# Optimization experiments

Measured on AMD Instinct MI355X. Metric: run time of the kernel, lower is better.

The kernel has to match this reference:

```python
import jax, jax.numpy as jnp
import numpy as np


def setup_inputs() -> dict:
    key = jax.random.key(0)
    x = jax.random.normal(key, (256, 64, 4096), dtype=jnp.float32)
    return {"x": x}


def _mat_shrinkage(cov, n):
    # cov: [B, p, p]; Rao-Blackwell Ledoit-Wolf shrinkage toward scaled identity
    p = cov.shape[-1]
    I = jnp.eye(p, dtype=cov.dtype)[None]                      # [1, p, p]
    trace = jnp.trace(cov, axis1=-2, axis2=-1)[:, None, None]  # [B, 1, 1]
    F_hat = trace / p * I                                      # [B, p, p]
    # tr(C @ C) without materializing C@C
    second_trace = jnp.einsum('bij,bji->b', cov, cov)[:, None, None]
    numerator = (n - 2) / n * second_trace + trace ** 2
    denominator = (n + 2) * (second_trace - trace ** 2 / p)
    rho = jnp.minimum(numerator / denominator, 1.0)
    return rho * F_hat + (1.0 - rho) * cov


def reference(x):
    # x: [B, C, M]
    B, C, M = x.shape
    x_mu = jnp.mean(x, axis=2, keepdims=True)          # [B, C, 1]
    x_cnt = x - x_mu                                    # [B, C, M]
    cov = jnp.einsum('bcm,bdm->bcd', x_cnt, x_cnt) / M  # [B, C, C]
    cov = _mat_shrinkage(cov, n=M)
    L = jnp.linalg.cholesky(jnp.linalg.inv(cov))        # [B, C, C], lower
    # Z = L^T @ x_cnt
    Z = jnp.einsum('bdc,bdm->bcm', L, x_cnt)            # [B, C, M]
    return Z
```

## Files before the change

### kernel.cpp

```cpp
#include <hip/hip_runtime.h>

#define B_ 256
#define C_ 64
#define M_ 4096

__global__ __launch_bounds__(256) void k_fused(const float* __restrict__ x,
                                               float* __restrict__ out) {
    const int b = blockIdx.x;
    const int t = threadIdx.x;
    const int w = t >> 6;
    const int l = t & 63;

    __shared__ float St[64][68];
    __shared__ float Cw[64][68];
    __shared__ float Ww[64][68];
    __shared__ float ms[64][17];
    __shared__ float mu[64];
    __shared__ float red[256];
    __shared__ float ucol[64];
    __shared__ float wmu[64];
    __shared__ float sc[4];

    const float* xb = x + (size_t)b * (C_ * M_);
    float* ob = out + (size_t)b * (C_ * M_);

    const int tc = l >> 3, td = l & 7;
    const int cl = l >> 2;
    const int m4 = l & 3;

    float acc[8][8];
#pragma unroll
    for (int i = 0; i < 8; ++i)
#pragma unroll
        for (int j = 0; j < 8; ++j) acc[i][j] = 0.f;
    float msum[4] = {0.f, 0.f, 0.f, 0.f};

    const int mbase = w * 1024;
    float4 r[4];
#pragma unroll
    for (int k = 0; k < 4; ++k)
        r[k] = *(const float4*)(xb + (size_t)(cl + 16 * k) * M_ + mbase + m4 * 4);

    for (int s = 0; s < 64; ++s) {
        __syncthreads();
#pragma unroll
        for (int k = 0; k < 4; ++k) {
            float4 v = r[k];
            msum[k] += v.x + v.y + v.z + v.w;
            const int row = w * 16 + m4 * 4;
            const int c = cl + 16 * k;
            St[row + 0][c] = v.x;
            St[row + 1][c] = v.y;
            St[row + 2][c] = v.z;
            St[row + 3][c] = v.w;
        }
        if (s < 63) {
#pragma unroll
            for (int k = 0; k < 4; ++k)
                r[k] = *(const float4*)(xb + (size_t)(cl + 16 * k) * M_ +
                                        mbase + (s + 1) * 16 + m4 * 4);
        }
        __syncthreads();
#pragma unroll 2
        for (int m = 0; m < 16; ++m) {
            float a[8], bb[8];
            *(float4*)&a[0]  = *(const float4*)&St[w * 16 + m][tc * 8];
            *(float4*)&a[4]  = *(const float4*)&St[w * 16 + m][tc * 8 + 4];
            *(float4*)&bb[0] = *(const float4*)&St[w * 16 + m][td * 8];
            *(float4*)&bb[4] = *(const float4*)&St[w * 16 + m][td * 8 + 4];
#pragma unroll
            for (int i = 0; i < 8; ++i)
#pragma unroll
                for (int j = 0; j < 8; ++j)
                    acc[i][j] = fmaf(a[i], bb[j], acc[i][j]);
        }
    }
#pragma unroll
    for (int k = 0; k < 4; ++k) ms[cl + 16 * k][w * 4 + m4] = msum[k];
    __syncthreads();

    if (w == 1) {
#pragma unroll
        for (int i = 0; i < 8; ++i) {
            *(float4*)&Ww[tc * 8 + i][td * 8]     = make_float4(acc[i][0], acc[i][1], acc[i][2], acc[i][3]);
            *(float4*)&Ww[tc * 8 + i][td * 8 + 4] = make_float4(acc[i][4], acc[i][5], acc[i][6], acc[i][7]);
        }
        float s = 0.f;
#pragma unroll
        for (int q = 0; q < 16; ++q) s += ms[l][q];
        mu[l] = s * (1.0f / M_);
    } else if (w == 2) {
#pragma unroll
        for (int i = 0; i < 8; ++i) {
            *(float4*)&Cw[tc * 8 + i][td * 8]     = make_float4(acc[i][0], acc[i][1], acc[i][2], acc[i][3]);
            *(float4*)&Cw[tc * 8 + i][td * 8 + 4] = make_float4(acc[i][4], acc[i][5], acc[i][6], acc[i][7]);
        }
    } else if (w == 3) {
#pragma unroll
        for (int i = 0; i < 8; ++i) {
            *(float4*)&St[tc * 8 + i][td * 8]     = make_float4(acc[i][0], acc[i][1], acc[i][2], acc[i][3]);
            *(float4*)&St[tc * 8 + i][td * 8 + 4] = make_float4(acc[i][4], acc[i][5], acc[i][6], acc[i][7]);
        }
    }
    __syncthreads();
    if (w == 0) {
#pragma unroll
        for (int i = 0; i < 8; ++i) {
            float4 p0 = *(const float4*)&Ww[tc * 8 + i][td * 8];
            float4 p1 = *(const float4*)&Cw[tc * 8 + i][td * 8];
            float4 p2 = *(const float4*)&St[tc * 8 + i][td * 8];
            float4 q0 = *(const float4*)&Ww[tc * 8 + i][td * 8 + 4];
            float4 q1 = *(const float4*)&Cw[tc * 8 + i][td * 8 + 4];
            float4 q2 = *(const float4*)&St[tc * 8 + i][td * 8 + 4];
            float4 lo = make_float4(acc[i][0] + p0.x + p1.x + p2.x,
                                    acc[i][1] + p0.y + p1.y + p2.y,
                                    acc[i][2] + p0.z + p1.z + p2.z,
                                    acc[i][3] + p0.w + p1.w + p2.w);
            float4 hi = make_float4(acc[i][4] + q0.x + q1.x + q2.x,
                                    acc[i][5] + q0.y + q1.y + q2.y,
                                    acc[i][6] + q0.z + q1.z + q2.z,
                                    acc[i][7] + q0.w + q1.w + q2.w);
            *(float4*)&Cw[tc * 8 + i][td * 8]     = lo;
            *(float4*)&Cw[tc * 8 + i][td * 8 + 4] = hi;
        }
    }
    __syncthreads();
    for (int idx = t; idx < 4096; idx += 256) {
        int i = idx >> 6, j = idx & 63;
        Cw[i][j] = Cw[i][j] * (1.0f / M_) - mu[i] * mu[j];
    }
    __syncthreads();

    {
        float trp = 0.f, stp = 0.f;
        for (int idx = t; idx < 4096; idx += 256) {
            int i = idx >> 6, j = idx & 63;
            float v = Cw[i][j];
            stp = fmaf(v, Cw[j][i], stp);
            if (i == j) trp += v;
        }
        red[t] = stp;
        __syncthreads();
        for (int off = 128; off > 0; off >>= 1) {
            if (t < off) red[t] += red[t + off];
            __syncthreads();
        }
        if (t == 0) sc[1] = red[0];
        __syncthreads();
        red[t] = trp;
        __syncthreads();
        for (int off = 128; off > 0; off >>= 1) {
            if (t < off) red[t] += red[t + off];
            __syncthreads();
        }
        if (t == 0) {
            float tr = red[0], st = sc[1];
            const float n = (float)M_, p = 64.f;
            float num = (n - 2.f) / n * st + tr * tr;
            float den = (n + 2.f) * (st - tr * tr / p);
            float rho = fminf(num / den, 1.0f);
            sc[0] = tr;
            sc[2] = rho;
        }
        __syncthreads();
        float rho = sc[2], tr = sc[0];
        float dadd = rho * tr * (1.0f / 64.0f);
        for (int idx = t; idx < 4096; idx += 256) {
            int i = idx >> 6, j = idx & 63;
            float v = (1.f - rho) * Cw[i][j];
            if (i == j) v += dadd;
            Cw[i][j] = v;
        }
    }

    for (int k = 63; k >= 0; --k) {
        __syncthreads();
        float dkk = sqrtf(Cw[k][k]);
        float dinv = 1.0f / dkk;
        for (int i = t; i < k; i += 256) ucol[i] = Cw[i][k] * dinv;
        if (t == 0) ucol[k] = dkk;
        __syncthreads();
        const int nel = (k * (k + 1)) >> 1;
        for (int e = t; e < nel; e += 256) {
            int j = (int)((sqrtf((float)(8 * e + 1)) - 1.0f) * 0.5f);
            if (e < ((j * (j + 1)) >> 1)) --j;
            else if (e >= (((j + 1) * (j + 2)) >> 1)) ++j;
            int i = e - ((j * (j + 1)) >> 1);
            Cw[i][j] = fmaf(-ucol[i], ucol[j], Cw[i][j]);
        }
        for (int i = t; i <= k; i += 256) Cw[i][k] = ucol[i];
    }
    __syncthreads();

    if (t < 64) {
        const int j = t;
        Ww[j][j] = 1.0f / Cw[j][j];
        for (int i = j - 1; i >= 0; --i) {
            float s0 = 0.f, s1 = 0.f;
            int lq = i + 1;
            for (; lq + 1 <= j; lq += 2) {
                s0 = fmaf(Cw[i][lq], Ww[lq][j], s0);
                s1 = fmaf(Cw[i][lq + 1], Ww[lq + 1][j], s1);
            }
            if (lq <= j) s0 = fmaf(Cw[i][lq], Ww[lq][j], s0);
            Ww[i][j] = -(s0 + s1) / Cw[i][i];
        }
    }
    __syncthreads();
    if (t < 64) {
        float s = 0.f;
        for (int d = t; d < 64; ++d) s = fmaf(Ww[t][d], mu[d], s);
        wmu[t] = s;
    }
    for (int idx = t; idx < 4096; idx += 256) {
        int d = idx >> 6, c = idx & 63;
        Cw[d][c] = (d >= c) ? Ww[c][d] : 0.f;
    }

    const int tc5 = t >> 5;
    const int tm5 = t & 31;
    const int cld = t >> 4;
    const int m45 = t & 15;
    const int d0 = w * 16;

    float4 r2[4];
#pragma unroll
    for (int k = 0; k < 4; ++k)
        r2[k] = *(const float4*)(xb + (size_t)(cld + 16 * k) * M_ + m45 * 4);

    for (int ch = 0; ch < 64; ++ch) {
        const int m0 = ch * 64;
        __syncthreads();
#pragma unroll
        for (int k = 0; k < 4; ++k)
            *(float4*)&St[cld + 16 * k][m45 * 4] = r2[k];
        if (ch < 63) {
#pragma unroll
            for (int k = 0; k < 4; ++k)
                r2[k] = *(const float4*)(xb + (size_t)(cld + 16 * k) * M_ +
                                         m0 + 64 + m45 * 4);
        }
        __syncthreads();
        float a2[8][2];
#pragma unroll
        for (int i = 0; i < 8; ++i) a2[i][0] = a2[i][1] = 0.f;
        for (int d = d0; d < 64; ++d) {
            float a[8];
            *(float4*)&a[0] = *(const float4*)&Cw[d][tc5 * 8];
            *(float4*)&a[4] = *(const float4*)&Cw[d][tc5 * 8 + 4];
            float2 bv = *(const float2*)&St[d][tm5 * 2];
#pragma unroll
            for (int i = 0; i < 8; ++i) {
                a2[i][0] = fmaf(a[i], bv.x, a2[i][0]);
                a2[i][1] = fmaf(a[i], bv.y, a2[i][1]);
            }
        }
#pragma unroll
        for (int i = 0; i < 8; ++i) {
            const int c = tc5 * 8 + i;
            float wv = wmu[c];
            float2 o = make_float2(a2[i][0] - wv, a2[i][1] - wv);
            *(float2*)(ob + (size_t)c * M_ + m0 + tm5 * 2) = o;
        }
    }
}

extern "C" void kernel_launch(void* const* d_in, const int* in_sizes, int n_in,
                              void* d_out, int out_size, void* d_ws, size_t ws_size,
                              hipStream_t stream) {
    const float* x = (const float*)d_in[0];
    float* out = (float*)d_out;
    k_fused<<<dim3(B_), 256, 0, stream>>>(x, out);
}
```

Before: 798.8 us.

## Split fused kernel into gram, cholesky and apply kernels with M-split parallelism

Replaces the single per-batch fused kernel with three kernels. The first computes raw Gram matrices and row sums over four M-slices per batch. The second reduces the slices, applies shrinkage, factors the matrix and inverts it. The third applies the triangular transform across four M-slices. This raises the grid from 256 blocks to 1024 blocks for the heavy phases so more CUs are busy, at the cost of a workspace round-trip, reading x twice and two extra launches. It also uses the uncentered Gram minus the mean outer product and folds the mean subtraction into a W·mu correction, which may lose some precision.

Result: faster. 749.2 us (-6.2%).

```diff
diff --git a/kernel.cpp b/kernel.cpp
--- a/kernel.cpp
+++ b/kernel.cpp
@@ -3,6 +3,340 @@
 #define B_ 256
 #define C_ 64
 #define M_ 4096
+#define S_ 4
+#define GSTRIDE 4160
+
+__global__ __launch_bounds__(256, 4) void k_gram(const float* __restrict__ x,
+                                                 float* __restrict__ wsA) {
+    const int b = blockIdx.x;
+    const int s = blockIdx.y;
+    const int t = threadIdx.x;
+    const int w = t >> 6;
+    const int l = t & 63;
+
+    __shared__ float St[64][68];
+    __shared__ float Bu[64][68];
+    __shared__ float ms[64][17];
+
+    const float* xb = x + (size_t)b * (C_ * M_);
+    float* g = wsA + (size_t)(b * S_ + s) * GSTRIDE;
+
+    const int tc = l >> 3, td = l & 7;
+    const int cl = l >> 2;
+    const int m4 = l & 3;
+
+    float acc[8][8];
+#pragma unroll
+    for (int i = 0; i < 8; ++i)
+#pragma unroll
+        for (int j = 0; j < 8; ++j) acc[i][j] = 0.f;
+    float msum[4] = {0.f, 0.f, 0.f, 0.f};
+
+    const int mbase = s * 1024 + w * 256;
+    float4 r[4];
+#pragma unroll
+    for (int k = 0; k < 4; ++k)
+        r[k] = *(const float4*)(xb + (size_t)(cl + 16 * k) * M_ + mbase + m4 * 4);
+
+    for (int st = 0; st < 16; ++st) {
+        __syncthreads();
+#pragma unroll
+        for (int k = 0; k < 4; ++k) {
+            float4 v = r[k];
+            msum[k] += v.x + v.y + v.z + v.w;
+            const int row = w * 16 + m4 * 4;
+            const int c = cl + 16 * k;
+            St[row + 0][c] = v.x;
+            St[row + 1][c] = v.y;
+            St[row + 2][c] = v.z;
+            St[row + 3][c] = v.w;
+        }
+        if (st < 15) {
+#pragma unroll
+            for (int k = 0; k < 4; ++k)
+                r[k] = *(const float4*)(xb + (size_t)(cl + 16 * k) * M_ +
+                                        mbase + (st + 1) * 16 + m4 * 4);
+        }
+        __syncthreads();
+#pragma unroll 2
+        for (int m = 0; m < 16; ++m) {
+            float a[8], bb[8];
+            *(float4*)&a[0]  = *(const float4*)&St[w * 16 + m][tc * 8];
+            *(float4*)&a[4]  = *(const float4*)&St[w * 16 + m][tc * 8 + 4];
+            *(float4*)&bb[0] = *(const float4*)&St[w * 16 + m][td * 8];
+            *(float4*)&bb[4] = *(const float4*)&St[w * 16 + m][td * 8 + 4];
+#pragma unroll
+            for (int i = 0; i < 8; ++i)
+#pragma unroll
+                for (int j = 0; j < 8; ++j)
+                    acc[i][j] = fmaf(a[i], bb[j], acc[i][j]);
+        }
+    }
+#pragma unroll
+    for (int k = 0; k < 4; ++k) ms[cl + 16 * k][w * 4 + m4] = msum[k];
+    __syncthreads();
+
+    if (w == 1) {
+#pragma unroll
+        for (int i = 0; i < 8; ++i) {
+            *(float4*)&St[tc * 8 + i][td * 8]     = make_float4(acc[i][0], acc[i][1], acc[i][2], acc[i][3]);
+            *(float4*)&St[tc * 8 + i][td * 8 + 4] = make_float4(acc[i][4], acc[i][5], acc[i][6], acc[i][7]);
+        }
+    } else if (w == 3) {
+#pragma unroll
+        for (int i = 0; i < 8; ++i) {
+            *(float4*)&Bu[tc * 8 + i][td * 8]     = make_float4(acc[i][0], acc[i][1], acc[i][2], acc[i][3]);
+            *(float4*)&Bu[tc * 8 + i][td * 8 + 4] = make_float4(acc[i][4], acc[i][5], acc[i][6], acc[i][7]);
+        }
+    }
+    __syncthreads();
+    if (w == 0) {
+#pragma unroll
+        for (int i = 0; i < 8; ++i) {
+            float4 p = *(const float4*)&St[tc * 8 + i][td * 8];
+            float4 q = *(const float4*)&St[tc * 8 + i][td * 8 + 4];
+            acc[i][0] += p.x; acc[i][1] += p.y; acc[i][2] += p.z; acc[i][3] += p.w;
+            acc[i][4] += q.x; acc[i][5] += q.y; acc[i][6] += q.z; acc[i][7] += q.w;
+        }
+    } else if (w == 2) {
+#pragma unroll
+        for (int i = 0; i < 8; ++i) {
+            float4 p = *(const float4*)&Bu[tc * 8 + i][td * 8];
+            float4 q = *(const float4*)&Bu[tc * 8 + i][td * 8 + 4];
+            acc[i][0] += p.x; acc[i][1] += p.y; acc[i][2] += p.z; acc[i][3] += p.w;
+            acc[i][4] += q.x; acc[i][5] += q.y; acc[i][6] += q.z; acc[i][7] += q.w;
+        }
+    }
+    __syncthreads();
+    if (w == 2) {
+#pragma unroll
+        for (int i = 0; i < 8; ++i) {
+            *(float4*)&St[tc * 8 + i][td * 8]     = make_float4(acc[i][0], acc[i][1], acc[i][2], acc[i][3]);
+            *(float4*)&St[tc * 8 + i][td * 8 + 4] = make_float4(acc[i][4], acc[i][5], acc[i][6], acc[i][7]);
+        }
+    }
+    __syncthreads();
+    if (w == 0) {
+#pragma unroll
+        for (int i = 0; i < 8; ++i) {
+            float4 p = *(const float4*)&St[tc * 8 + i][td * 8];
+            float4 q = *(const float4*)&St[tc * 8 + i][td * 8 + 4];
+            float4 lo = make_float4(acc[i][0] + p.x, acc[i][1] + p.y,
+                                    acc[i][2] + p.z, acc[i][3] + p.w);
+            float4 hi = make_float4(acc[i][4] + q.x, acc[i][5] + q.y,
+                                    acc[i][6] + q.z, acc[i][7] + q.w);
+            *(float4*)(g + (size_t)(tc * 8 + i) * 64 + td * 8)     = lo;
+            *(float4*)(g + (size_t)(tc * 8 + i) * 64 + td * 8 + 4) = hi;
+        }
+    } else if (w == 1) {
+        float sum = 0.f;
+#pragma unroll
+        for (int q = 0; q < 16; ++q) sum += ms[l][q];
+        g[4096 + l] = sum;
+    }
+}
+
+__global__ __launch_bounds__(256) void k_chol(const float* __restrict__ wsA,
+                                              float* __restrict__ wsB) {
+    const int b = blockIdx.x;
+    const int t = threadIdx.x;
+
+    __shared__ float Cw[64][68];
+    __shared__ float Ww[64][68];
+    __shared__ float mu[64];
+    __shared__ float red[256];
+    __shared__ float ucol[64];
+    __shared__ float sc[4];
+
+    const float* pa = wsA + (size_t)b * S_ * GSTRIDE;
+    float* o = wsB + (size_t)b * GSTRIDE;
+
+    for (int idx = t; idx < 4096; idx += 256) {
+        float v = 0.f;
+#pragma unroll
+        for (int s = 0; s < S_; ++s) v += pa[(size_t)s * GSTRIDE + idx];
+        Cw[idx >> 6][idx & 63] = v;
+    }
+    if (t < 64) {
+        float v = 0.f;
+#pragma unroll
+        for (int s = 0; s < S_; ++s) v += pa[(size_t)s * GSTRIDE + 4096 + t];
+        mu[t] = v * (1.0f / M_);
+    }
+    __syncthreads();
+    for (int idx = t; idx < 4096; idx += 256) {
+        int i = idx >> 6, j = idx & 63;
+        Cw[i][j] = Cw[i][j] * (1.0f / M_) - mu[i] * mu[j];
+    }
+    __syncthreads();
+
+    {
+        float trp = 0.f, stp = 0.f;
+        for (int idx = t; idx < 4096; idx += 256) {
+            int i = idx >> 6, j = idx & 63;
+            float v = Cw[i][j];
+            stp = fmaf(v, Cw[j][i], stp);
+            if (i == j) trp += v;
+        }
+        red[t] = stp;
+        __syncthreads();
+        for (int off = 128; off > 0; off >>= 1) {
+            if (t < off) red[t] += red[t + off];
+            __syncthreads();
+        }
+        if (t == 0) sc[1] = red[0];
+        __syncthreads();
+        red[t] = trp;
+        __syncthreads();
+        for (int off = 128; off > 0; off >>= 1) {
+            if (t < off) red[t] += red[t + off];
+            __syncthreads();
+        }
+        if (t == 0) {
+            float tr = red[0], st = sc[1];
+            const float n = (float)M_, p = 64.f;
+            float num = (n - 2.f) / n * st + tr * tr;
+            float den = (n + 2.f) * (st - tr * tr / p);
+            float rho = fminf(num / den, 1.0f);
+            sc[0] = tr;
+            sc[2] = rho;
+        }
+        __syncthreads();
+        float rho = sc[2], tr = sc[0];
+        float dadd = rho * tr * (1.0f / 64.0f);
+        for (int idx = t; idx < 4096; idx += 256) {
+            int i = idx >> 6, j = idx & 63;
+            float v = (1.f - rho) * Cw[i][j];
+            if (i == j) v += dadd;
+            Cw[i][j] = v;
+        }
+    }
+
+    for (int k = 63; k >= 0; --k) {
+        __syncthreads();
+        float dkk = sqrtf(Cw[k][k]);
+        float dinv = 1.0f / dkk;
+        for (int i = t; i < k; i += 256) ucol[i] = Cw[i][k] * dinv;
+        if (t == 0) ucol[k] = dkk;
+        __syncthreads();
+        const int nel = (k * (k + 1)) >> 1;
+        for (int e = t; e < nel; e += 256) {
+            int j = (int)((sqrtf((float)(8 * e + 1)) - 1.0f) * 0.5f);
+            if (e < ((j * (j + 1)) >> 1)) --j;
+            else if (e >= (((j + 1) * (j + 2)) >> 1)) ++j;
+            int i = e - ((j * (j + 1)) >> 1);
+            Cw[i][j] = fmaf(-ucol[i], ucol[j], Cw[i][j]);
+        }
+        for (int i = t; i <= k; i += 256) Cw[i][k] = ucol[i];
+    }
+    __syncthreads();
+
+    if (t < 64) {
+        const int j = t;
+        Ww[j][j] = 1.0f / Cw[j][j];
+        for (int i = j - 1; i >= 0; --i) {
+            float s0 = 0.f, s1 = 0.f;
+            int lq = i + 1;
+            for (; lq + 1 <= j; lq += 2) {
+                s0 = fmaf(Cw[i][lq], Ww[lq][j], s0);
+                s1 = fmaf(Cw[i][lq + 1], Ww[lq + 1][j], s1);
+            }
+            if (lq <= j) s0 = fmaf(Cw[i][lq], Ww[lq][j], s0);
+            Ww[i][j] = -(s0 + s1) / Cw[i][i];
+        }
+    }
+    __syncthreads();
+    if (t < 64) {
+        float s = 0.f;
+        for (int d = t; d < 64; ++d) s = fmaf(Ww[t][d], mu[d], s);
+        o[4096 + t] = s;
+    }
+    for (int idx = t; idx < 4096; idx += 256) {
+        int d = idx >> 6, c = idx & 63;
+        o[idx] = (d >= c) ? Ww[c][d] : 0.f;
+    }
+}
+
+__global__ __launch_bounds__(256, 4) void k_apply(const float* __restrict__ x,
+                                                  const float* __restrict__ wsB,
+                                                  float* __restrict__ out) {
+    const int b = blockIdx.x;
+    const int s = blockIdx.y;
+    const int t = threadIdx.x;
+    const int w = t >> 6;
+
+    __shared__ float Wt[64][68];
+    __shared__ float St[64][68];
+    __shared__ float wmu[64];
+
+    const float* xb = x + (size_t)b * (C_ * M_);
+    float* ob = out + (size_t)b * (C_ * M_);
+    const float* wsb = wsB + (size_t)b * GSTRIDE;
+
+    for (int idx = t; idx < 4096; idx += 256) Wt[idx >> 6][idx & 63] = wsb[idx];
+    if (t < 64) wmu[t] = wsb[4096 + t];
+
+    const int tc5 = t >> 4;
+    const int tm5 = t & 15;
+    const int cld = t >> 4;
+    const int m45 = t & 15;
+    const int d0 = w * 16;
+    const int mbase = s * 1024;
+
+    float4 r2[4];
+#pragma unroll
+    for (int k = 0; k < 4; ++k)
+        r2[k] = *(const float4*)(xb + (size_t)(cld + 16 * k) * M_ + mbase + m45 * 4);
+
+    for (int ch = 0; ch < 16; ++ch) {
+        const int m0 = mbase + ch * 64;
+        __syncthreads();
+#pragma unroll
+        for (int k = 0; k < 4; ++k)
+            *(float4*)&St[cld + 16 * k][m45 * 4] = r2[k];
+        if (ch < 15) {
+#pragma unroll
+            for (int k = 0; k < 4; ++k)
+                r2[k] = *(const float4*)(xb + (size_t)(cld + 16 * k) * M_ +
+                                         m0 + 64 + m45 * 4);
+        }
+        __syncthreads();
+        float a2[4][4];
+#pragma unroll
+        for (int i = 0; i < 4; ++i)
+#pragma unroll
+            for (int j = 0; j < 4; ++j) a2[i][j] = 0.f;
+#pragma unroll 2
+        for (int d = d0; d < 64; ++d) {
+            float4 a  = *(const float4*)&Wt[d][tc5 * 4];
+            float4 bv = *(const float4*)&St[d][tm5 * 4];
+            a2[0][0] = fmaf(a.x, bv.x, a2[0][0]);
+            a2[0][1] = fmaf(a.x, bv.y, a2[0][1]);
+            a2[0][2] = fmaf(a.x, bv.z, a2[0][2]);
+            a2[0][3] = fmaf(a.x, bv.w, a2[0][3]);
+            a2[1][0] = fmaf(a.y, bv.x, a2[1][0]);
+            a2[1][1] = fmaf(a.y, bv.y, a2[1][1]);
+            a2[1][2] = fmaf(a.y, bv.z, a2[1][2]);
+            a2[1][3] = fmaf(a.y, bv.w, a2[1][3]);
+            a2[2][0] = fmaf(a.z, bv.x, a2[2][0]);
+            a2[2][1] = fmaf(a.z, bv.y, a2[2][1]);
+            a2[2][2] = fmaf(a.z, bv.z, a2[2][2]);
+            a2[2][3] = fmaf(a.z, bv.w, a2[2][3]);
+            a2[3][0] = fmaf(a.w, bv.x, a2[3][0]);
+            a2[3][1] = fmaf(a.w, bv.y, a2[3][1]);
+            a2[3][2] = fmaf(a.w, bv.z, a2[3][2]);
+            a2[3][3] = fmaf(a.w, bv.w, a2[3][3]);
+        }
+#pragma unroll
+        for (int i = 0; i < 4; ++i) {
+            const int c = tc5 * 4 + i;
+            float wv = wmu[c];
+            float4 o = make_float4(a2[i][0] - wv, a2[i][1] - wv,
+                                   a2[i][2] - wv, a2[i][3] - wv);
+            *(float4*)(ob + (size_t)c * M_ + m0 + tm5 * 4) = o;
+        }
+    }
+}
 
 __global__ __launch_bounds__(256) void k_fused(const float* __restrict__ x,
                                                float* __restrict__ out) {
@@ -270,5 +604,14 @@
                               hipStream_t stream) {
     const float* x = (const float*)d_in[0];
     float* out = (float*)d_out;
-    k_fused<<<dim3(B_), 256, 0, stream>>>(x, out);
+    const size_t needed = (size_t)(B_ * S_ + B_) * GSTRIDE * sizeof(float);
+    if (d_ws && ws_size >= needed) {
+        float* wsA = (float*)d_ws;
+        float* wsB = wsA + (size_t)B_ * S_ * GSTRIDE;
+        k_gram<<<dim3(B_, S_), 256, 0, stream>>>(x, wsA);
+        k_chol<<<dim3(B_), 256, 0, stream>>>(wsA, wsB);
+        k_apply<<<dim3(B_, S_), 256, 0, stream>>>(x, wsB, out);
+    } else {
+        k_fused<<<dim3(B_), 256, 0, stream>>>(x, out);
+    }
 }
```
